# Optimization experiments

Measured on AMD Instinct MI355X. Metric: run time of the kernel, lower is better.

The kernel has to match this reference:

```python
import jax, jax.numpy as jnp
import numpy as np

N_NODES = 100000
N_EDGES = 1638400
IN_CH = 128
HEADS = 4
OUT_CH = 32


def setup_inputs() -> dict:
    key = jax.random.key(0)
    ks = jax.random.split(key, 7)
    x = jax.random.normal(ks[0], (N_NODES, IN_CH), dtype=jnp.float32)
    W = jax.random.normal(ks[1], (HEADS * OUT_CH, IN_CH), dtype=jnp.float32) * (1.0 / np.sqrt(IN_CH))
    b = jax.random.normal(ks[2], (HEADS * OUT_CH,), dtype=jnp.float32) * 0.01
    att_l = jax.random.normal(ks[3], (1, HEADS, OUT_CH), dtype=jnp.float32) * 0.1
    att_r = jax.random.normal(ks[4], (1, HEADS, OUT_CH), dtype=jnp.float32) * 0.1
    src_idx = jax.random.randint(ks[5], (N_EDGES,), 0, N_NODES, dtype=jnp.int32)
    trg_idx = jax.random.randint(ks[6], (N_EDGES,), 0, N_NODES, dtype=jnp.int32)
    return {"x": x, "W": W, "b": b, "att_l": att_l, "att_r": att_r,
            "src_idx": src_idx, "trg_idx": trg_idx}


def reference(x, W, b, att_l, att_r, src_idx, trg_idx):
    # linear projection: [N, in] -> [N, H, C]
    h = (x @ W.T + b).reshape(-1, HEADS, OUT_CH)
    # per-node attention scores: [N, H]
    alpha_l = jnp.sum(att_l * h, axis=-1)
    alpha_r = jnp.sum(att_r * h, axis=-1)
    # lift: edge-wise gathers, [E, H] and [E, H, C]
    alpha_lifted = alpha_l[src_idx] + alpha_r[trg_idx]
    alpha_per_edge = jax.nn.leaky_relu(alpha_lifted, negative_slope=0.01)
    x_lifted = h[src_idx]
    return alpha_per_edge, x_lifted
```

## Files before the change

### kernel.cpp

```cpp
#include <hip/hip_runtime.h>
#include <hip/hip_bf16.h>

#define N_NODES 100000
#define N_EDGES 1638400
#define IN_CH   128
#define HEADS   4
#define OUT_CH  32
#define HC      (HEADS * OUT_CH)

__launch_bounds__(256)
__global__ void gat_gemm_kernel(const float* __restrict__ x,
                                const float* __restrict__ W,
                                const float* __restrict__ bias,
                                float* __restrict__ h, int n) {
    __shared__ float sWt[128 * 129];
    __shared__ float sX[64 * 128];

    const int t = threadIdx.x;
    const int node_base = blockIdx.x * 64;

    #pragma unroll 4
    for (int i = 0; i < 64; ++i) {
        int idx = i * 256 + t;
        int o = idx >> 7, k = idx & 127;
        sWt[k * 129 + o] = W[idx];
    }

    {
        const float4* x4 = (const float4*)(x + (size_t)node_base * IN_CH);
        float4* sX4 = (float4*)sX;
        int rows = n - node_base;
        for (int i = t; i < 64 * 32; i += 256) {
            int row = i >> 5;
            float4 v = make_float4(0.f, 0.f, 0.f, 0.f);
            if (row < rows) v = x4[i];
            sX4[i] = v;
        }
    }
    __syncthreads();

    const int c = t & 31;
    const int g = t >> 5;

    float acc[8][4];
    #pragma unroll
    for (int i = 0; i < 8; ++i)
        #pragma unroll
        for (int j = 0; j < 4; ++j) acc[i][j] = 0.f;

    #pragma unroll 4
    for (int k = 0; k < 128; ++k) {
        float w0 = sWt[k * 129 + c];
        float w1 = sWt[k * 129 + c + 32];
        float w2 = sWt[k * 129 + c + 64];
        float w3 = sWt[k * 129 + c + 96];
        #pragma unroll
        for (int i = 0; i < 8; ++i) {
            float xv = sX[(g * 8 + i) * 128 + k];
            acc[i][0] += xv * w0;
            acc[i][1] += xv * w1;
            acc[i][2] += xv * w2;
            acc[i][3] += xv * w3;
        }
    }

    const float b0 = bias[c], b1 = bias[c + 32], b2 = bias[c + 64], b3 = bias[c + 96];
    #pragma unroll
    for (int i = 0; i < 8; ++i) {
        int node = node_base + g * 8 + i;
        if (node < n) {
            float* hp = h + (size_t)node * HC;
            hp[c]      = acc[i][0] + b0;
            hp[c + 32] = acc[i][1] + b1;
            hp[c + 64] = acc[i][2] + b2;
            hp[c + 96] = acc[i][3] + b3;
        }
    }
}

__launch_bounds__(256)
__global__ void gat_alpha_kernel(const float* __restrict__ h,
                                 const float* __restrict__ att_l,
                                 const float* __restrict__ att_r,
                                 float* __restrict__ al,
                                 float* __restrict__ ar, int n) {
    int idx = blockIdx.x * 256 + threadIdx.x;
    if (idx >= n * HEADS) return;
    int node = idx >> 2, head = idx & 3;
    const float4* hp = (const float4*)(h + (size_t)node * HC + head * OUT_CH);
    const float4* lp = (const float4*)(att_l + head * OUT_CH);
    const float4* rp = (const float4*)(att_r + head * OUT_CH);
    float sl = 0.f, sr = 0.f;
    #pragma unroll
    for (int j = 0; j < 8; ++j) {
        float4 v = hp[j], l = lp[j], r = rp[j];
        sl += v.x * l.x + v.y * l.y + v.z * l.z + v.w * l.w;
        sr += v.x * r.x + v.y * r.y + v.z * r.z + v.w * r.w;
    }
    al[idx] = sl;
    ar[idx] = sr;
}

__launch_bounds__(256)
__global__ void gat_edge_kernel(const int* __restrict__ src_idx,
                                const int* __restrict__ trg_idx,
                                const float* __restrict__ h,
                                const float* __restrict__ al,
                                const float* __restrict__ ar,
                                float* __restrict__ out_alpha,
                                float* __restrict__ out_x) {
    int tid = blockIdx.x * 256 + threadIdx.x;
    int e = tid >> 5;
    int lane = tid & 31;
    if (e >= N_EDGES) return;

    int src = src_idx[e];

    float4 v = *(const float4*)(h + (size_t)src * HC + lane * 4);
    *(float4*)(out_x + (size_t)e * HC + lane * 4) = v;

    if (lane == 0) {
        int trg = trg_idx[e];
        float4 a = *(const float4*)(al + (size_t)src * HEADS);
        float4 b = *(const float4*)(ar + (size_t)trg * HEADS);
        float4 o;
        float s;
        s = a.x + b.x; o.x = s > 0.f ? s : 0.01f * s;
        s = a.y + b.y; o.y = s > 0.f ? s : 0.01f * s;
        s = a.z + b.z; o.z = s > 0.f ? s : 0.01f * s;
        s = a.w + b.w; o.w = s > 0.f ? s : 0.01f * s;
        *(float4*)(out_alpha + (size_t)e * HEADS) = o;
    }
}

extern "C" void kernel_launch(void* const* d_in, const int* in_sizes, int n_in,
                              void* d_out, int out_size, void* d_ws, size_t ws_size,
                              hipStream_t stream) {
    const float* x     = (const float*)d_in[0];
    const float* W     = (const float*)d_in[1];
    const float* bias  = (const float*)d_in[2];
    const float* att_l = (const float*)d_in[3];
    const float* att_r = (const float*)d_in[4];
    const int* src_idx = (const int*)d_in[5];
    const int* trg_idx = (const int*)d_in[6];

    float* h  = (float*)d_ws;
    float* al = h + (size_t)N_NODES * HC;
    float* ar = al + (size_t)N_NODES * HEADS;

    float* out_alpha = (float*)d_out;
    float* out_x     = out_alpha + (size_t)N_EDGES * HEADS;

    int gemm_blocks = (N_NODES + 63) / 64;
    gat_gemm_kernel<<<gemm_blocks, 256, 0, stream>>>(x, W, bias, h, N_NODES);

    int alpha_blocks = (N_NODES * HEADS + 255) / 256;
    gat_alpha_kernel<<<alpha_blocks, 256, 0, stream>>>(h, att_l, att_r, al, ar, N_NODES);

    int edge_blocks = (N_EDGES * 32) / 256;
    gat_edge_kernel<<<edge_blocks, 256, 0, stream>>>(src_idx, trg_idx, h, al, ar,
                                                     out_alpha, out_x);
}
```

Before: 1.183 ms.

## Fuse attention-score reduction into GEMM epilogue, halve W smem, nontemporal edge I/O

The per-node attention dot products are now computed in the GEMM epilogue with wave shuffles, which removes the separate alpha kernel and its re-read of h. The transposed W tile in shared memory is split into two 64-row K-chunks so the block uses less LDS, and launch bounds now ask for 2 blocks per SM. The edge gather kernel uses nontemporal loads for the indices and nontemporal stores for its large outputs to avoid polluting cache. The cost is an extra W reload and barrier per K-chunk, plus shuffle work in the epilogue.

```diff
diff --git a/kernel.cpp b/kernel.cpp
--- a/kernel.cpp
+++ b/kernel.cpp
@@ -1,5 +1,4 @@
 #include <hip/hip_runtime.h>
-#include <hip/hip_bf16.h>
 
 #define N_NODES 100000
 #define N_EDGES 1638400
@@ -8,39 +7,36 @@
 #define OUT_CH  32
 #define HC      (HEADS * OUT_CH)
 
-__launch_bounds__(256)
+typedef float f4 __attribute__((ext_vector_type(4)));
+
+__launch_bounds__(256, 2)
 __global__ void gat_gemm_kernel(const float* __restrict__ x,
                                 const float* __restrict__ W,
                                 const float* __restrict__ bias,
-                                float* __restrict__ h, int n) {
-    __shared__ float sWt[128 * 129];
+                                const float* __restrict__ att_l,
+                                const float* __restrict__ att_r,
+                                float* __restrict__ h,
+                                float* __restrict__ al,
+                                float* __restrict__ ar, int n) {
+    __shared__ float sWt[64 * 129];
     __shared__ float sX[64 * 128];
 
     const int t = threadIdx.x;
     const int node_base = blockIdx.x * 64;
-
-    #pragma unroll 4
-    for (int i = 0; i < 64; ++i) {
-        int idx = i * 256 + t;
-        int o = idx >> 7, k = idx & 127;
-        sWt[k * 129 + o] = W[idx];
-    }
+    const int c = t & 31;
+    const int g = t >> 5;
 
     {
-        const float4* x4 = (const float4*)(x + (size_t)node_base * IN_CH);
-        float4* sX4 = (float4*)sX;
+        const f4* x4 = (const f4*)(x + (size_t)node_base * IN_CH);
+        f4* sX4 = (f4*)sX;
         int rows = n - node_base;
         for (int i = t; i < 64 * 32; i += 256) {
             int row = i >> 5;
-            float4 v = make_float4(0.f, 0.f, 0.f, 0.f);
+            f4 v = {0.f, 0.f, 0.f, 0.f};
             if (row < rows) v = x4[i];
             sX4[i] = v;
         }
     }
-    __syncthreads();
-
-    const int c = t & 31;
-    const int g = t >> 5;
 
     float acc[8][4];
     #pragma unroll
@@ -48,57 +44,79 @@
         #pragma unroll
         for (int j = 0; j < 4; ++j) acc[i][j] = 0.f;
 
-    #pragma unroll 4
-    for (int k = 0; k < 128; ++k) {
-        float w0 = sWt[k * 129 + c];
-        float w1 = sWt[k * 129 + c + 32];
-        float w2 = sWt[k * 129 + c + 64];
-        float w3 = sWt[k * 129 + c + 96];
+    const f4* W4 = (const f4*)W;
+
+    for (int kb = 0; kb < 128; kb += 64) {
+        __syncthreads();
+
         #pragma unroll
         for (int i = 0; i < 8; ++i) {
-            float xv = sX[(g * 8 + i) * 128 + k];
-            acc[i][0] += xv * w0;
-            acc[i][1] += xv * w1;
-            acc[i][2] += xv * w2;
-            acc[i][3] += xv * w3;
+            int idx = i * 256 + t;
+            int o = idx >> 4, j = idx & 15;
+            f4 w = W4[o * 32 + (kb >> 2) + j];
+            sWt[(4 * j + 0) * 129 + o] = w.x;
+            sWt[(4 * j + 1) * 129 + o] = w.y;
+            sWt[(4 * j + 2) * 129 + o] = w.z;
+            sWt[(4 * j + 3) * 129 + o] = w.w;
+        }
+        __syncthreads();
+
+        #pragma unroll 4
+        for (int kl = 0; kl < 64; ++kl) {
+            int k = kb + kl;
+            float w0 = sWt[kl * 129 + c];
+            float w1 = sWt[kl * 129 + c + 32];
+            float w2 = sWt[kl * 129 + c + 64];
+            float w3 = sWt[kl * 129 + c + 96];
+            #pragma unroll
+            for (int i = 0; i < 8; ++i) {
+                float xv = sX[(g * 8 + i) * 128 + k];
+                acc[i][0] += xv * w0;
+                acc[i][1] += xv * w1;
+                acc[i][2] += xv * w2;
+                acc[i][3] += xv * w3;
+            }
         }
     }
 
     const float b0 = bias[c], b1 = bias[c + 32], b2 = bias[c + 64], b3 = bias[c + 96];
+    const float l0 = att_l[c], l1 = att_l[c + 32], l2 = att_l[c + 64], l3 = att_l[c + 96];
+    const float r0 = att_r[c], r1 = att_r[c + 32], r2 = att_r[c + 64], r3 = att_r[c + 96];
+
     #pragma unroll
     for (int i = 0; i < 8; ++i) {
         int node = node_base + g * 8 + i;
+        float h0 = acc[i][0] + b0;
+        float h1 = acc[i][1] + b1;
+        float h2 = acc[i][2] + b2;
+        float h3 = acc[i][3] + b3;
         if (node < n) {
             float* hp = h + (size_t)node * HC;
-            hp[c]      = acc[i][0] + b0;
-            hp[c + 32] = acc[i][1] + b1;
-            hp[c + 64] = acc[i][2] + b2;
-            hp[c + 96] = acc[i][3] + b3;
+            hp[c]      = h0;
+            hp[c + 32] = h1;
+            hp[c + 64] = h2;
+            hp[c + 96] = h3;
+        }
+        float pl0 = l0 * h0, pl1 = l1 * h1, pl2 = l2 * h2, pl3 = l3 * h3;
+        float pr0 = r0 * h0, pr1 = r1 * h1, pr2 = r2 * h2, pr3 = r3 * h3;
+        #pragma unroll
+        for (int off = 16; off; off >>= 1) {
+            pl0 += __shfl_xor(pl0, off);
+            pl1 += __shfl_xor(pl1, off);
+            pl2 += __shfl_xor(pl2, off);
+            pl3 += __shfl_xor(pl3, off);
+            pr0 += __shfl_xor(pr0, off);
+            pr1 += __shfl_xor(pr1, off);
+            pr2 += __shfl_xor(pr2, off);
+            pr3 += __shfl_xor(pr3, off);
+        }
+        if (c == 0 && node < n) {
+            f4 va = {pl0, pl1, pl2, pl3};
+            f4 vb = {pr0, pr1, pr2, pr3};
+            *(f4*)(al + (size_t)node * HEADS) = va;
+            *(f4*)(ar + (size_t)node * HEADS) = vb;
         }
     }
-}
-
-__launch_bounds__(256)
-__global__ void gat_alpha_kernel(const float* __restrict__ h,
-                                 const float* __restrict__ att_l,
-                                 const float* __restrict__ att_r,
-                                 float* __restrict__ al,
-                                 float* __restrict__ ar, int n) {
-    int idx = blockIdx.x * 256 + threadIdx.x;
-    if (idx >= n * HEADS) return;
-    int node = idx >> 2, head = idx & 3;
-    const float4* hp = (const float4*)(h + (size_t)node * HC + head * OUT_CH);
-    const float4* lp = (const float4*)(att_l + head * OUT_CH);
-    const float4* rp = (const float4*)(att_r + head * OUT_CH);
-    float sl = 0.f, sr = 0.f;
-    #pragma unroll
-    for (int j = 0; j < 8; ++j) {
-        float4 v = hp[j], l = lp[j], r = rp[j];
-        sl += v.x * l.x + v.y * l.y + v.z * l.z + v.w * l.w;
-        sr += v.x * r.x + v.y * r.y + v.z * r.z + v.w * r.w;
-    }
-    al[idx] = sl;
-    ar[idx] = sr;
 }
 
 __launch_bounds__(256)
@@ -112,24 +130,23 @@
     int tid = blockIdx.x * 256 + threadIdx.x;
     int e = tid >> 5;
     int lane = tid & 31;
-    if (e >= N_EDGES) return;
 
-    int src = src_idx[e];
+    int src = __builtin_nontemporal_load(src_idx + e);
 
-    float4 v = *(const float4*)(h + (size_t)src * HC + lane * 4);
-    *(float4*)(out_x + (size_t)e * HC + lane * 4) = v;
+    f4 v = *(const f4*)(h + (size_t)src * HC + lane * 4);
+    __builtin_nontemporal_store(v, (f4*)(out_x + (size_t)e * HC + lane * 4));
 
     if (lane == 0) {
-        int trg = trg_idx[e];
-        float4 a = *(const float4*)(al + (size_t)src * HEADS);
-        float4 b = *(const float4*)(ar + (size_t)trg * HEADS);
-        float4 o;
+        int trg = __builtin_nontemporal_load(trg_idx + e);
+        f4 a = *(const f4*)(al + (size_t)src * HEADS);
+        f4 b = *(const f4*)(ar + (size_t)trg * HEADS);
+        f4 o;
         float s;
         s = a.x + b.x; o.x = s > 0.f ? s : 0.01f * s;
         s = a.y + b.y; o.y = s > 0.f ? s : 0.01f * s;
         s = a.z + b.z; o.z = s > 0.f ? s : 0.01f * s;
         s = a.w + b.w; o.w = s > 0.f ? s : 0.01f * s;
-        *(float4*)(out_alpha + (size_t)e * HEADS) = o;
+        __builtin_nontemporal_store(o, (f4*)(out_alpha + (size_t)e * HEADS));
     }
 }
 
@@ -152,10 +169,8 @@
     float* out_x     = out_alpha + (size_t)N_EDGES * HEADS;
 
     int gemm_blocks = (N_NODES + 63) / 64;
-    gat_gemm_kernel<<<gemm_blocks, 256, 0, stream>>>(x, W, bias, h, N_NODES);
-
-    int alpha_blocks = (N_NODES * HEADS + 255) / 256;
-    gat_alpha_kernel<<<alpha_blocks, 256, 0, stream>>>(h, att_l, att_r, al, ar, N_NODES);
+    gat_gemm_kernel<<<gemm_blocks, 256, 0, stream>>>(x, W, bias, att_l, att_r,
+                                                     h, al, ar, N_NODES);
 
     int edge_blocks = (N_EDGES * 32) / 256;
     gat_edge_kernel<<<edge_blocks, 256, 0, stream>>>(src_idx, trg_idx, h, al, ar,
```

Measured after the change: 1.151 ms. 1.03x faster.
